# Optimization experiments

Measured on AMD Instinct MI355X. Metric: run time of the kernel, lower is better.

Reference implementation:

```python
import jax, jax.numpy as jnp
import numpy as np

NUM_USERS = 100000
NUM_ITEMS = 50000
N = NUM_USERS + NUM_ITEMS
E = 3000000
DIM = 64


def setup_inputs() -> dict:
    key = jax.random.key(0)
    ks = jax.random.split(key, 8)
    emb_users = 0.01 * jax.random.normal(ks[0], (NUM_USERS, DIM), dtype=jnp.float32)
    emb_items = 0.01 * jax.random.normal(ks[1], (NUM_ITEMS, DIM), dtype=jnp.float32)
    # GCNConv linear weights (bias separate, as in PyG: lin(bias=False) + bias param)
    s = 1.0 / np.sqrt(DIM)
    W1 = jax.random.uniform(ks[2], (DIM, DIM), jnp.float32, -s, s)
    b1 = jnp.zeros((DIM,), jnp.float32)
    W2 = jax.random.uniform(ks[3], (DIM, DIM), jnp.float32, -s, s)
    b2 = jnp.zeros((DIM,), jnp.float32)
    edge_index = jax.random.randint(ks[4], (2, E), 0, N, dtype=jnp.int64)
    edge_weight = jax.random.uniform(ks[5], (E,), jnp.float32)
    return {"emb_users": emb_users, "emb_items": emb_items,
            "W1": W1, "b1": b1, "W2": W2, "b2": b2,
            "edge_index": edge_index, "edge_weight": edge_weight}


def _gcn_conv(x, W, b, row, col):
    """PyG GCNConv with add_self_loops=True, improved=False, unit edge weights.
    out[i] = sum_{j->i} d_j^-1/2 d_i^-1/2 (x_j W) + d_i^-1 (x_i W) + b
    where d includes the self-loop (+1).
    """
    n = x.shape[0]
    xw = x @ W                                           # [N, D]
    deg = jax.ops.segment_sum(jnp.ones_like(row, dtype=x.dtype), col,
                              num_segments=n) + 1.0      # in-degree + self-loop
    dinv = jax.lax.rsqrt(deg)                            # [N]
    coef = dinv[row] * dinv[col]                         # [E]
    msg = xw[row] * coef[:, None]                        # gather + scale  [E, D]
    out = jax.ops.segment_sum(msg, col, num_segments=n)  # scatter-add     [N, D]
    out = out + xw * (dinv * dinv)[:, None]              # self-loop term
    return out + b


def reference(emb_users, emb_items, W1, b1, W2, b2, edge_index, edge_weight):
    # edge_weight is accepted by forward() but never passed to the GCN convs
    row, col = edge_index[0], edge_index[1]
    emb = jnp.concatenate([emb_users, emb_items], axis=0)  # [N, D]
    embs = [emb]
    for W, b in ((W1, b1), (W2, b2)):
        emb = _gcn_conv(emb, W, b, row, col)
        embs.append(emb)
        emb = jax.nn.relu(emb)
    return jnp.stack(embs)  # [num_layers+1, N, D]
```

## Files before the change

### kernel.cpp

```cpp
#include <hip/hip_runtime.h>
#include <hip/hip_fp16.h>

#define DIM 64
#define BPN 1024
#define ECHUNK 8192
#define MAXNB 160

typedef _Float16 f16x8 __attribute__((ext_vector_type(8)));
typedef float f32x4 __attribute__((ext_vector_type(4)));


__global__ __launch_bounds__(1024) void bucket_count_kernel(
    const int* __restrict__ col, int* __restrict__ bucket_cnt, int E, int NB) {
  __shared__ int h[MAXNB];
  for (int t = threadIdx.x; t < NB; t += blockDim.x) h[t] = 0;
  __syncthreads();
  int base = blockIdx.x * ECHUNK;
  int end = min(base + ECHUNK, E);
  for (int e = base + (int)threadIdx.x; e < end; e += blockDim.x)
    atomicAdd(&h[col[e] >> 10], 1);
  __syncthreads();
  for (int t = threadIdx.x; t < NB; t += blockDim.x)
    if (h[t]) atomicAdd(&bucket_cnt[t], h[t]);
}

__global__ __launch_bounds__(256) void bucket_scan_kernel(
    const int* __restrict__ bucket_cnt, int* __restrict__ bucket_base,
    int* __restrict__ bucket_cursor, int* __restrict__ off, int NB, int N, int E) {
  __shared__ int wsum[4];
  __shared__ int woff[4];
  const int t = threadIdx.x;
  const int lane = t & 63, wid = t >> 6;
  int v = (t < NB) ? bucket_cnt[t] : 0;
  int x = v;
#pragma unroll
  for (int d = 1; d < 64; d <<= 1) {
    int s = __shfl_up(x, d, 64);
    if (lane >= d) x += s;
  }
  if (lane == 63) wsum[wid] = x;
  __syncthreads();
  if (t == 0) {
    int s = 0;
#pragma unroll
    for (int k = 0; k < 4; k++) { woff[k] = s; s += wsum[k]; }
  }
  __syncthreads();
  int excl = woff[wid] + x - v;
  if (t < NB) { bucket_base[t] = excl; bucket_cursor[t] = excl; }
  if (t == 0) {
    bucket_base[NB] = woff[3] + wsum[3];
    off[N] = E;
  }
}

__global__ __launch_bounds__(1024) void bucket_scatter_kernel(
    const int* __restrict__ row, const int* __restrict__ col,
    int* __restrict__ bucket_cursor, int* __restrict__ packed, int E, int NB) {
  __shared__ int h[MAXNB];
  __shared__ int excl0[MAXNB];
  __shared__ int cur[MAXNB];
  __shared__ int gbase[MAXNB];
  __shared__ int wsum[16];
  __shared__ int woff[16];
  __shared__ int staging[ECHUNK];
  __shared__ unsigned short map[ECHUNK];
  const int tid = threadIdx.x;
  for (int t = tid; t < NB; t += blockDim.x) h[t] = 0;
  __syncthreads();
  int base = blockIdx.x * ECHUNK;
  int end = min(base + ECHUNK, E);
  int total = end - base;
  for (int e = base + tid; e < end; e += blockDim.x)
    atomicAdd(&h[col[e] >> 10], 1);
  __syncthreads();
  {
    const int lane = tid & 63, wid = tid >> 6;
    int v = (tid < NB) ? h[tid] : 0;
    int x = v;
#pragma unroll
    for (int d = 1; d < 64; d <<= 1) {
      int s = __shfl_up(x, d, 64);
      if (lane >= d) x += s;
    }
    if (lane == 63) wsum[wid] = x;
    __syncthreads();
    if (tid == 0) {
      int s = 0;
#pragma unroll
      for (int k = 0; k < 16; k++) { woff[k] = s; s += wsum[k]; }
    }
    __syncthreads();
    if (tid < NB) {
      int excl = woff[wid] + x - v;
      excl0[tid] = excl;
      cur[tid] = excl;
    }
  }
  __syncthreads();
  if (tid < NB) {
    if (h[tid] > 0) gbase[tid] = atomicAdd(&bucket_cursor[tid], h[tid]);
    int s = excl0[tid], c = h[tid];
    for (int j = 0; j < c; j++) map[s + j] = (unsigned short)tid;
  }
  __syncthreads();
  for (int e = base + tid; e < end; e += blockDim.x) {
    int c = col[e];
    int b = c >> 10;
    int pos = atomicAdd(&cur[b], 1);
    staging[pos] = ((c & (BPN - 1)) << 18) | row[e];
  }
  __syncthreads();
  for (int idx = tid; idx < total; idx += blockDim.x) {
    int b = map[idx];
    packed[gbase[b] + idx - excl0[b]] = staging[idx];
  }
}

__global__ __launch_bounds__(1024) void bucket_csr_kernel(
    const int* __restrict__ packed, const int* __restrict__ bucket_base,
    int* __restrict__ perm_row, int* __restrict__ off, float* __restrict__ dinv, int N) {
  __shared__ int nh[BPN];
  __shared__ int ncur[BPN];
  __shared__ int wsum[16];
  __shared__ int woff[16];
  const int b = blockIdx.x;
  const int tid = threadIdx.x;
  const int ebase = bucket_base[b];
  const int cnt = bucket_base[b + 1] - ebase;
  nh[tid] = 0;
  __syncthreads();
  for (int i = tid; i < cnt; i += 1024)
    atomicAdd(&nh[packed[ebase + i] >> 18], 1);
  __syncthreads();
  const int lane = tid & 63, wid = tid >> 6;
  int v = nh[tid], x = v;
#pragma unroll
  for (int d = 1; d < 64; d <<= 1) {
    int t = __shfl_up(x, d, 64);
    if (lane >= d) x += t;
  }
  if (lane == 63) wsum[wid] = x;
  __syncthreads();
  if (tid == 0) {
    int s = 0;
#pragma unroll
    for (int k = 0; k < 16; k++) { woff[k] = s; s += wsum[k]; }
  }
  __syncthreads();
  int excl = woff[wid] + x - v;
  ncur[tid] = excl;
  int node = b * BPN + tid;
  if (node < N) {
    off[node] = ebase + excl;
    dinv[node] = rsqrtf((float)v + 1.0f);
  }
  __syncthreads();
  for (int i = tid; i < cnt; i += 1024) {
    int p = packed[ebase + i];
    int local = p >> 18;
    int pos = atomicAdd(&ncur[local], 1);
    perm_row[ebase + pos] = p & 0x3FFFF;
  }
}

__global__ __launch_bounds__(256) void edge_coef_kernel(
    const int* __restrict__ perm_row, const float* __restrict__ dinv,
    int2* __restrict__ edata, int E) {
  int e = blockIdx.x * 256 + threadIdx.x;
  if (e >= E) return;
  int r = perm_row[e];
  edata[e] = make_int2(r, __float_as_int(dinv[r]));
}

__global__ __launch_bounds__(256) void xw_mfma_kernel(
    const float* __restrict__ xa, const float* __restrict__ xb,
    const float* __restrict__ W, float* __restrict__ out0,
    __half* __restrict__ xwh, int NU, int N, int do_relu) {
  __shared__ _Float16 Wt[64 * 72];
  for (int t = threadIdx.x; t < 4096; t += 256) {
    int k = t >> 6, n = t & 63;
    Wt[n * 72 + k] = (_Float16)W[t];
  }
  __syncthreads();
  const int lane = threadIdx.x & 63;
  const int wid = threadIdx.x >> 6;
  const int m = lane & 15;
  const int quad = lane >> 4;
  f16x8 bfrag[4][2];
#pragma unroll
  for (int c = 0; c < 4; c++)
#pragma unroll
    for (int s = 0; s < 2; s++)
      bfrag[c][s] = *(const f16x8*)&Wt[(c * 16 + m) * 72 + s * 32 + quad * 8];

  const int rbase = (blockIdx.x * 4 + wid) * 16;
  if (rbase >= N) return;
  const int r = rbase + m;
  const int rr = min(r, N - 1);
  const float* src = (xb == nullptr || rr < NU) ? xa + (size_t)rr * DIM
                                                : xb + (size_t)(rr - NU) * DIM;
  f16x8 afrag[2];
#pragma unroll
  for (int s = 0; s < 2; s++) {
    float4 u0 = *(const float4*)(src + s * 32 + quad * 8);
    float4 u1 = *(const float4*)(src + s * 32 + quad * 8 + 4);
    if (out0 != nullptr && r < N) {
      float4* o = (float4*)(out0 + (size_t)r * DIM);
      o[s * 8 + quad * 2] = u0;
      o[s * 8 + quad * 2 + 1] = u1;
    }
    if (do_relu) {
      u0.x = fmaxf(u0.x, 0.f); u0.y = fmaxf(u0.y, 0.f);
      u0.z = fmaxf(u0.z, 0.f); u0.w = fmaxf(u0.w, 0.f);
      u1.x = fmaxf(u1.x, 0.f); u1.y = fmaxf(u1.y, 0.f);
      u1.z = fmaxf(u1.z, 0.f); u1.w = fmaxf(u1.w, 0.f);
    }
    afrag[s][0] = (_Float16)u0.x; afrag[s][1] = (_Float16)u0.y;
    afrag[s][2] = (_Float16)u0.z; afrag[s][3] = (_Float16)u0.w;
    afrag[s][4] = (_Float16)u1.x; afrag[s][5] = (_Float16)u1.y;
    afrag[s][6] = (_Float16)u1.z; afrag[s][7] = (_Float16)u1.w;
  }
  f32x4 acc[4];
#pragma unroll
  for (int c = 0; c < 4; c++) {
    acc[c] = (f32x4){0.f, 0.f, 0.f, 0.f};
    acc[c] = __builtin_amdgcn_mfma_f32_16x16x32_f16(afrag[0], bfrag[c][0], acc[c], 0, 0, 0);
    acc[c] = __builtin_amdgcn_mfma_f32_16x16x32_f16(afrag[1], bfrag[c][1], acc[c], 0, 0, 0);
  }
#pragma unroll
  for (int reg = 0; reg < 4; reg++) {
    int orow = rbase + quad * 4 + reg;
    if (orow < N) {
      __half* dst = xwh + (size_t)orow * DIM + m;
#pragma unroll
      for (int c = 0; c < 4; c++)
        dst[c * 16] = __float2half(acc[c][reg]);
    }
  }
}

__global__ void aggregate_kernel(const __half* __restrict__ xwh, const int* __restrict__ off,
                                 const int2* __restrict__ edata, const float* __restrict__ dinv,
                                 const float* __restrict__ b, float* __restrict__ out,
                                 int nbase, int ncnt) {
  const int lane = threadIdx.x & 63;
  const int li = blockIdx.x * (blockDim.x >> 6) + (threadIdx.x >> 6);
  if (li >= ncnt) return;
  const int i = nbase + li;
  const int esel = lane >> 3;
  const int j = lane & 7;
  const float di = dinv[i];
  const float4* rows = (const float4*)xwh;
  float acc[8];
#pragma unroll
  for (int q = 0; q < 8; q++) acc[q] = 0.0f;
  if (esel == 0) {
    float4 f = rows[(size_t)i * 8 + j];
    const __half2* h = (const __half2*)&f;
#pragma unroll
    for (int q = 0; q < 4; q++) {
      float2 p = __half22float2(h[q]);
      acc[2 * q] = di * p.x;
      acc[2 * q + 1] = di * p.y;
    }
  }
  const int s0 = off[i], s1 = off[i + 1];
  const int last = s1 - 1;
  for (int k = s0; k < s1; k += 32) {
    const int e0 = k + esel, e1 = e0 + 8, e2 = e0 + 16, e3 = e0 + 24;
    int2 v0 = edata[min(e0, last)];
    int2 v1 = edata[min(e1, last)];
    int2 v2 = edata[min(e2, last)];
    int2 v3 = edata[min(e3, last)];
    float c0 = (e0 <= last) ? __int_as_float(v0.y) : 0.0f;
    float c1 = (e1 <= last) ? __int_as_float(v1.y) : 0.0f;
    float c2 = (e2 <= last) ? __int_as_float(v2.y) : 0.0f;
    float c3 = (e3 <= last) ? __int_as_float(v3.y) : 0.0f;
    float4 f0 = rows[(size_t)v0.x * 8 + j];
    float4 f1 = rows[(size_t)v1.x * 8 + j];
    float4 f2 = rows[(size_t)v2.x * 8 + j];
    float4 f3 = rows[(size_t)v3.x * 8 + j];
    const __half2* h0 = (const __half2*)&f0;
    const __half2* h1 = (const __half2*)&f1;
    const __half2* h2 = (const __half2*)&f2;
    const __half2* h3 = (const __half2*)&f3;
#pragma unroll
    for (int q = 0; q < 4; q++) {
      float2 p0 = __half22float2(h0[q]);
      acc[2 * q] += c0 * p0.x;
      acc[2 * q + 1] += c0 * p0.y;
    }
#pragma unroll
    for (int q = 0; q < 4; q++) {
      float2 p1 = __half22float2(h1[q]);
      acc[2 * q] += c1 * p1.x;
      acc[2 * q + 1] += c1 * p1.y;
    }
#pragma unroll
    for (int q = 0; q < 4; q++) {
      float2 p2 = __half22float2(h2[q]);
      acc[2 * q] += c2 * p2.x;
      acc[2 * q + 1] += c2 * p2.y;
    }
#pragma unroll
    for (int q = 0; q < 4; q++) {
      float2 p3 = __half22float2(h3[q]);
      acc[2 * q] += c3 * p3.x;
      acc[2 * q + 1] += c3 * p3.y;
    }
  }
#pragma unroll
  for (int q = 0; q < 8; q++) {
    acc[q] += __shfl_xor(acc[q], 8, 64);
    acc[q] += __shfl_xor(acc[q], 16, 64);
    acc[q] += __shfl_xor(acc[q], 32, 64);
  }
  if (esel == 0) {
    float4 b0 = ((const float4*)b)[2 * j];
    float4 b1 = ((const float4*)b)[2 * j + 1];
    float4* orow = (float4*)(out + (size_t)i * DIM);
    orow[2 * j] = make_float4(di * acc[0] + b0.x, di * acc[1] + b0.y,
                              di * acc[2] + b0.z, di * acc[3] + b0.w);
    orow[2 * j + 1] = make_float4(di * acc[4] + b1.x, di * acc[5] + b1.y,
                                  di * acc[6] + b1.z, di * acc[7] + b1.w);
  }
}

extern "C" void kernel_launch(void* const* d_in, const int* in_sizes, int n_in,
                              void* d_out, int out_size, void* d_ws, size_t ws_size,
                              hipStream_t stream) {
  const float* emb_users = (const float*)d_in[0];
  const float* emb_items = (const float*)d_in[1];
  const float* W1 = (const float*)d_in[2];
  const float* b1 = (const float*)d_in[3];
  const float* W2 = (const float*)d_in[4];
  const float* b2 = (const float*)d_in[5];
  const int* edge_index = (const int*)d_in[6];

  const int NU = in_sizes[0] / DIM;
  const int NI = in_sizes[1] / DIM;
  const int N = NU + NI;
  const int E = in_sizes[6] / 2;
  const int NB = (N + BPN - 1) / BPN;
  const int* row = edge_index;
  const int* col = edge_index + E;

  float* out = (float*)d_out;

  char* ws = (char*)d_ws;
  size_t o = 0;
  auto alloc = [&](size_t bytes) -> void* {
    o = (o + 255) & ~(size_t)255;
    void* p = ws + o;
    o += bytes;
    return p;
  };
  int* bucket_cnt    = (int*)alloc((size_t)NB * 4);
  int* bucket_base   = (int*)alloc((size_t)(NB + 1) * 4);
  int* bucket_cursor = (int*)alloc((size_t)NB * 4);
  int* off           = (int*)alloc((size_t)(N + 1) * 4);
  float* dinv        = (float*)alloc((size_t)N * 4);
  int* perm_row      = (int*)alloc((size_t)E * 4);
  int2* edata        = (int2*)alloc((size_t)E * 8);
  __half* xwh        = (__half*)alloc((size_t)N * DIM * 2);
  int* packed        = (int*)xwh;
  (void)ws_size;

  const int nbE = (E + ECHUNK - 1) / ECHUNK;

  hipMemsetAsync(bucket_cnt, 0, (size_t)NB * 4, stream);
  bucket_count_kernel<<<nbE, 1024, 0, stream>>>(col, bucket_cnt, E, NB);
  bucket_scan_kernel<<<1, 256, 0, stream>>>(bucket_cnt, bucket_base, bucket_cursor, off, NB, N, E);
  bucket_scatter_kernel<<<nbE, 1024, 0, stream>>>(row, col, bucket_cursor, packed, E, NB);
  bucket_csr_kernel<<<NB, 1024, 0, stream>>>(packed, bucket_base, perm_row, off, dinv, N);
  edge_coef_kernel<<<(E + 255) / 256, 256, 0, stream>>>(perm_row, dinv, edata, E);

  const int TB = 256;
  const int gx = (N + 63) / 64;
  const int NH = (N + 1) / 2;
  const int g1 = (NH + 3) / 4;
  const int g2 = (N - NH + 3) / 4;

  xw_mfma_kernel<<<gx, TB, 0, stream>>>(emb_users, emb_items, W1, out, xwh, NU, N, 0);
  aggregate_kernel<<<g1, TB, 0, stream>>>((const __half*)xwh, off, edata, dinv, b1,
                                          out + (size_t)N * DIM, 0, NH);
  aggregate_kernel<<<g2, TB, 0, stream>>>((const __half*)xwh, off, edata, dinv, b1,
                                          out + (size_t)N * DIM, NH, N - NH);

  xw_mfma_kernel<<<gx, TB, 0, stream>>>(out + (size_t)N * DIM, nullptr, W2, nullptr, xwh, N, N, 1);
  aggregate_kernel<<<g1, TB, 0, stream>>>((const __half*)xwh, off, edata, dinv, b2,
                                          out + (size_t)2 * N * DIM, 0, NH);
  aggregate_kernel<<<g2, TB, 0, stream>>>((const __half*)xwh, off, edata, dinv, b2,
                                          out + (size_t)2 * N * DIM, NH, N - NH);
}
```

Before: 404.4 us.

## Replace two-level bucket CSR build with global atomic histogram and scatter

Swaps the bucketed two-pass CSR construction (per-chunk shared histograms, staging, per-bucket local sort) for a direct build: a global atomic degree histogram, a three-kernel prefix scan, and a scatter that uses a global atomic cursor per destination node. The scatter also writes the edge's row index and dinv directly, which removes the separate perm_row pass and edge_coef kernel. The cost is 3M global atomics on random addresses twice, plus random scattered writes of edata, in place of the locality-friendly bucket passes. Edge order within each node becomes nondeterministic, so float summation order can vary between runs.

```diff
diff --git a/kernel.cpp b/kernel.cpp
--- a/kernel.cpp
+++ b/kernel.cpp
@@ -2,41 +2,62 @@
 #include <hip/hip_fp16.h>
 
 #define DIM 64
-#define BPN 1024
-#define ECHUNK 8192
-#define MAXNB 160
 
 typedef _Float16 f16x8 __attribute__((ext_vector_type(8)));
 typedef float f32x4 __attribute__((ext_vector_type(4)));
 
 
-__global__ __launch_bounds__(1024) void bucket_count_kernel(
-    const int* __restrict__ col, int* __restrict__ bucket_cnt, int E, int NB) {
-  __shared__ int h[MAXNB];
-  for (int t = threadIdx.x; t < NB; t += blockDim.x) h[t] = 0;
-  __syncthreads();
-  int base = blockIdx.x * ECHUNK;
-  int end = min(base + ECHUNK, E);
-  for (int e = base + (int)threadIdx.x; e < end; e += blockDim.x)
-    atomicAdd(&h[col[e] >> 10], 1);
-  __syncthreads();
-  for (int t = threadIdx.x; t < NB; t += blockDim.x)
-    if (h[t]) atomicAdd(&bucket_cnt[t], h[t]);
-}
-
-__global__ __launch_bounds__(256) void bucket_scan_kernel(
-    const int* __restrict__ bucket_cnt, int* __restrict__ bucket_base,
-    int* __restrict__ bucket_cursor, int* __restrict__ off, int NB, int N, int E) {
+__global__ __launch_bounds__(256) void deg_hist_kernel(
+    const int* __restrict__ col, int* __restrict__ deg, int E) {
+  const int stride = gridDim.x * 256;
+  for (int e = blockIdx.x * 256 + threadIdx.x; e < E; e += stride)
+    atomicAdd(&deg[col[e]], 1);
+}
+
+__global__ __launch_bounds__(1024) void deg_scan_local_kernel(
+    const int* __restrict__ deg, int* __restrict__ exoff,
+    int* __restrict__ bsum, float* __restrict__ dinv, int N) {
+  __shared__ int wsum[16];
+  __shared__ int woff[16];
+  const int tid = threadIdx.x;
+  const int node = blockIdx.x * 1024 + tid;
+  const int d = (node < N) ? deg[node] : 0;
+  const int lane = tid & 63, wid = tid >> 6;
+  int x = d;
+#pragma unroll
+  for (int s = 1; s < 64; s <<= 1) {
+    int t = __shfl_up(x, s, 64);
+    if (lane >= s) x += t;
+  }
+  if (lane == 63) wsum[wid] = x;
+  __syncthreads();
+  if (tid == 0) {
+    int s = 0;
+#pragma unroll
+    for (int k = 0; k < 16; k++) { woff[k] = s; s += wsum[k]; }
+  }
+  __syncthreads();
+  const int incl = woff[wid] + x;
+  if (node < N) {
+    exoff[node] = incl - d;
+    dinv[node] = rsqrtf((float)d + 1.0f);
+  }
+  if (tid == 1023) bsum[blockIdx.x] = incl;
+}
+
+__global__ __launch_bounds__(256) void deg_scan_blocks_kernel(
+    const int* __restrict__ bsum, int* __restrict__ bbase,
+    int* __restrict__ off, int NBLK, int N, int E) {
   __shared__ int wsum[4];
   __shared__ int woff[4];
   const int t = threadIdx.x;
   const int lane = t & 63, wid = t >> 6;
-  int v = (t < NB) ? bucket_cnt[t] : 0;
+  int v = (t < NBLK) ? bsum[t] : 0;
   int x = v;
 #pragma unroll
-  for (int d = 1; d < 64; d <<= 1) {
-    int s = __shfl_up(x, d, 64);
-    if (lane >= d) x += s;
+  for (int s = 1; s < 64; s <<= 1) {
+    int u = __shfl_up(x, s, 64);
+    if (lane >= s) x += u;
   }
   if (lane == 63) wsum[wid] = x;
   __syncthreads();
@@ -46,131 +67,32 @@
     for (int k = 0; k < 4; k++) { woff[k] = s; s += wsum[k]; }
   }
   __syncthreads();
-  int excl = woff[wid] + x - v;
-  if (t < NB) { bucket_base[t] = excl; bucket_cursor[t] = excl; }
-  if (t == 0) {
-    bucket_base[NB] = woff[3] + wsum[3];
-    off[N] = E;
-  }
-}
-
-__global__ __launch_bounds__(1024) void bucket_scatter_kernel(
+  if (t < NBLK) bbase[t] = woff[wid] + x - v;
+  if (t == 0) off[N] = E;
+}
+
+__global__ __launch_bounds__(1024) void deg_scan_final_kernel(
+    const int* __restrict__ exoff, const int* __restrict__ bbase,
+    int* __restrict__ off, int* __restrict__ cursor, int N) {
+  const int node = blockIdx.x * 1024 + threadIdx.x;
+  if (node < N) {
+    const int o = bbase[blockIdx.x] + exoff[node];
+    off[node] = o;
+    cursor[node] = o;
+  }
+}
+
+__global__ __launch_bounds__(256) void edge_scatter_kernel(
     const int* __restrict__ row, const int* __restrict__ col,
-    int* __restrict__ bucket_cursor, int* __restrict__ packed, int E, int NB) {
-  __shared__ int h[MAXNB];
-  __shared__ int excl0[MAXNB];
-  __shared__ int cur[MAXNB];
-  __shared__ int gbase[MAXNB];
-  __shared__ int wsum[16];
-  __shared__ int woff[16];
-  __shared__ int staging[ECHUNK];
-  __shared__ unsigned short map[ECHUNK];
-  const int tid = threadIdx.x;
-  for (int t = tid; t < NB; t += blockDim.x) h[t] = 0;
-  __syncthreads();
-  int base = blockIdx.x * ECHUNK;
-  int end = min(base + ECHUNK, E);
-  int total = end - base;
-  for (int e = base + tid; e < end; e += blockDim.x)
-    atomicAdd(&h[col[e] >> 10], 1);
-  __syncthreads();
-  {
-    const int lane = tid & 63, wid = tid >> 6;
-    int v = (tid < NB) ? h[tid] : 0;
-    int x = v;
-#pragma unroll
-    for (int d = 1; d < 64; d <<= 1) {
-      int s = __shfl_up(x, d, 64);
-      if (lane >= d) x += s;
-    }
-    if (lane == 63) wsum[wid] = x;
-    __syncthreads();
-    if (tid == 0) {
-      int s = 0;
-#pragma unroll
-      for (int k = 0; k < 16; k++) { woff[k] = s; s += wsum[k]; }
-    }
-    __syncthreads();
-    if (tid < NB) {
-      int excl = woff[wid] + x - v;
-      excl0[tid] = excl;
-      cur[tid] = excl;
-    }
-  }
-  __syncthreads();
-  if (tid < NB) {
-    if (h[tid] > 0) gbase[tid] = atomicAdd(&bucket_cursor[tid], h[tid]);
-    int s = excl0[tid], c = h[tid];
-    for (int j = 0; j < c; j++) map[s + j] = (unsigned short)tid;
-  }
-  __syncthreads();
-  for (int e = base + tid; e < end; e += blockDim.x) {
-    int c = col[e];
-    int b = c >> 10;
-    int pos = atomicAdd(&cur[b], 1);
-    staging[pos] = ((c & (BPN - 1)) << 18) | row[e];
-  }
-  __syncthreads();
-  for (int idx = tid; idx < total; idx += blockDim.x) {
-    int b = map[idx];
-    packed[gbase[b] + idx - excl0[b]] = staging[idx];
-  }
-}
-
-__global__ __launch_bounds__(1024) void bucket_csr_kernel(
-    const int* __restrict__ packed, const int* __restrict__ bucket_base,
-    int* __restrict__ perm_row, int* __restrict__ off, float* __restrict__ dinv, int N) {
-  __shared__ int nh[BPN];
-  __shared__ int ncur[BPN];
-  __shared__ int wsum[16];
-  __shared__ int woff[16];
-  const int b = blockIdx.x;
-  const int tid = threadIdx.x;
-  const int ebase = bucket_base[b];
-  const int cnt = bucket_base[b + 1] - ebase;
-  nh[tid] = 0;
-  __syncthreads();
-  for (int i = tid; i < cnt; i += 1024)
-    atomicAdd(&nh[packed[ebase + i] >> 18], 1);
-  __syncthreads();
-  const int lane = tid & 63, wid = tid >> 6;
-  int v = nh[tid], x = v;
-#pragma unroll
-  for (int d = 1; d < 64; d <<= 1) {
-    int t = __shfl_up(x, d, 64);
-    if (lane >= d) x += t;
-  }
-  if (lane == 63) wsum[wid] = x;
-  __syncthreads();
-  if (tid == 0) {
-    int s = 0;
-#pragma unroll
-    for (int k = 0; k < 16; k++) { woff[k] = s; s += wsum[k]; }
-  }
-  __syncthreads();
-  int excl = woff[wid] + x - v;
-  ncur[tid] = excl;
-  int node = b * BPN + tid;
-  if (node < N) {
-    off[node] = ebase + excl;
-    dinv[node] = rsqrtf((float)v + 1.0f);
-  }
-  __syncthreads();
-  for (int i = tid; i < cnt; i += 1024) {
-    int p = packed[ebase + i];
-    int local = p >> 18;
-    int pos = atomicAdd(&ncur[local], 1);
-    perm_row[ebase + pos] = p & 0x3FFFF;
-  }
-}
-
-__global__ __launch_bounds__(256) void edge_coef_kernel(
-    const int* __restrict__ perm_row, const float* __restrict__ dinv,
+    const float* __restrict__ dinv, int* __restrict__ cursor,
     int2* __restrict__ edata, int E) {
-  int e = blockIdx.x * 256 + threadIdx.x;
-  if (e >= E) return;
-  int r = perm_row[e];
-  edata[e] = make_int2(r, __float_as_int(dinv[r]));
+  const int stride = gridDim.x * 256;
+  for (int e = blockIdx.x * 256 + threadIdx.x; e < E; e += stride) {
+    const int c = col[e];
+    const int r = row[e];
+    const int pos = atomicAdd(&cursor[c], 1);
+    edata[pos] = make_int2(r, __float_as_int(dinv[r]));
+  }
 }
 
 __global__ __launch_bounds__(256) void xw_mfma_kernel(
@@ -342,7 +264,6 @@
   const int NI = in_sizes[1] / DIM;
   const int N = NU + NI;
   const int E = in_sizes[6] / 2;
-  const int NB = (N + BPN - 1) / BPN;
   const int* row = edge_index;
   const int* col = edge_index + E;
 
@@ -356,25 +277,24 @@
     o += bytes;
     return p;
   };
-  int* bucket_cnt    = (int*)alloc((size_t)NB * 4);
-  int* bucket_base   = (int*)alloc((size_t)(NB + 1) * 4);
-  int* bucket_cursor = (int*)alloc((size_t)NB * 4);
-  int* off           = (int*)alloc((size_t)(N + 1) * 4);
-  float* dinv        = (float*)alloc((size_t)N * 4);
-  int* perm_row      = (int*)alloc((size_t)E * 4);
-  int2* edata        = (int2*)alloc((size_t)E * 8);
-  __half* xwh        = (__half*)alloc((size_t)N * DIM * 2);
-  int* packed        = (int*)xwh;
+  const int NBLK = (N + 1023) / 1024;
+  int* deg     = (int*)alloc((size_t)N * 4);
+  int* exoff   = (int*)alloc((size_t)N * 4);
+  int* bsum    = (int*)alloc(256 * 4);
+  int* bbase   = (int*)alloc(256 * 4);
+  int* off     = (int*)alloc((size_t)(N + 1) * 4);
+  int* cursor  = (int*)alloc((size_t)N * 4);
+  float* dinv  = (float*)alloc((size_t)N * 4);
+  int2* edata  = (int2*)alloc((size_t)E * 8);
+  __half* xwh  = (__half*)alloc((size_t)N * DIM * 2);
   (void)ws_size;
 
-  const int nbE = (E + ECHUNK - 1) / ECHUNK;
-
-  hipMemsetAsync(bucket_cnt, 0, (size_t)NB * 4, stream);
-  bucket_count_kernel<<<nbE, 1024, 0, stream>>>(col, bucket_cnt, E, NB);
-  bucket_scan_kernel<<<1, 256, 0, stream>>>(bucket_cnt, bucket_base, bucket_cursor, off, NB, N, E);
-  bucket_scatter_kernel<<<nbE, 1024, 0, stream>>>(row, col, bucket_cursor, packed, E, NB);
-  bucket_csr_kernel<<<NB, 1024, 0, stream>>>(packed, bucket_base, perm_row, off, dinv, N);
-  edge_coef_kernel<<<(E + 255) / 256, 256, 0, stream>>>(perm_row, dinv, edata, E);
+  hipMemsetAsync(deg, 0, (size_t)N * 4, stream);
+  deg_hist_kernel<<<2048, 256, 0, stream>>>(col, deg, E);
+  deg_scan_local_kernel<<<NBLK, 1024, 0, stream>>>(deg, exoff, bsum, dinv, N);
+  deg_scan_blocks_kernel<<<1, 256, 0, stream>>>(bsum, bbase, off, NBLK, N, E);
+  deg_scan_final_kernel<<<NBLK, 1024, 0, stream>>>(exoff, bbase, off, cursor, N);
+  edge_scatter_kernel<<<2048, 256, 0, stream>>>(row, col, dinv, cursor, edata, E);
 
   const int TB = 256;
   const int gx = (N + 63) / 64;
```

Measured after the change: 588.5 us. 45.5% more time.
